# Kernel tuning notes

Measured on AMD Instinct MI355X. Metric: run time of the kernel, lower is better.

The kernel has to match this reference:

```python
import jax, jax.numpy as jnp
import numpy as np

N, E, F_IN, G = 50000, 800000, 128, 256
LAYERS = [(128, 4, 64), (256, 4, 64), (256, 1, 64)]  # (fan_in, heads, per-head dim)


def setup_inputs() -> dict:
    key = jax.random.key(0)
    ks = iter(jax.random.split(key, 64))
    nrm = lambda shp, s=1.0: jax.random.normal(next(ks), shp, jnp.float32) * s
    d = {}
    d["x"] = nrm((N, F_IN))
    d["edge_index"] = jax.random.randint(next(ks), (2, E), 0, N, dtype=jnp.int32)
    d["batch"] = jnp.sort(jax.random.randint(next(ks), (N,), 0, G, dtype=jnp.int32))
    for i, (fin, h, c) in enumerate(LAYERS):
        d[f"w{i}"] = nrm((fin, h * c), 1.0 / np.sqrt(fin))
        d[f"asrc{i}"] = nrm((h, c), 0.1)
        d[f"adst{i}"] = nrm((h, c), 0.1)
        d[f"b{i}"] = nrm((h * c,), 0.1)
        d[f"g{i}"] = 1.0 + nrm((h * c,), 0.1)
        d[f"be{i}"] = nrm((h * c,), 0.1)
        d[f"m{i}"] = nrm((h * c,), 0.1)
        d[f"v{i}"] = jnp.abs(nrm((h * c,), 0.1)) + 1.0
    d["fc1w"] = nrm((192, 64), 1.0 / np.sqrt(192)); d["fc1b"] = nrm((64,), 0.1)
    d["fc2w"] = nrm((64, 32), 1.0 / np.sqrt(64));   d["fc2b"] = nrm((32,), 0.1)
    d["fc3w"] = nrm((32, 1), 1.0 / np.sqrt(32));    d["fc3b"] = nrm((1,), 0.1)
    return d


def _gat_layer(x, w, a_s, a_d, b, src, dst, n, heads):
    c = w.shape[1] // heads
    h = (x @ w).reshape(n, heads, c)                      # [N,H,C]
    al_s = jnp.sum(h * a_s[None], axis=-1)                # [N,H]
    al_d = jnp.sum(h * a_d[None], axis=-1)                # [N,H]
    e = jax.nn.leaky_relu(al_s[src] + al_d[dst], 0.2)     # [E',H]
    emax = jax.ops.segment_max(e, dst, num_segments=n)
    emax = jnp.where(jnp.isfinite(emax), emax, 0.0)
    ee = jnp.exp(e - emax[dst])
    den = jax.ops.segment_sum(ee, dst, num_segments=n)
    alpha = ee / (den[dst] + 1e-16)                       # edge softmax per dst node
    out = jax.ops.segment_sum(h[src] * alpha[..., None], dst, num_segments=n)
    return out.reshape(n, heads * c) + b


def _bn(x, g, be, m, v):
    return (x - m) * jax.lax.rsqrt(v + 1e-5) * g + be


def reference(x, edge_index, batch,
              w0, asrc0, adst0, b0, g0, be0, m0, v0,
              w1, asrc1, adst1, b1, g1, be1, m1, v1,
              w2, asrc2, adst2, b2, g2, be2, m2, v2,
              fc1w, fc1b, fc2w, fc2b, fc3w, fc3b):
    n = x.shape[0]
    loop = jnp.arange(n, dtype=edge_index.dtype)          # add_self_loops (PyG default)
    src = jnp.concatenate([edge_index[0], loop])
    dst = jnp.concatenate([edge_index[1], loop])
    layers = [(w0, asrc0, adst0, b0, g0, be0, m0, v0, 4),
              (w1, asrc1, adst1, b1, g1, be1, m1, v1, 4),
              (w2, asrc2, adst2, b2, g2, be2, m2, v2, 1)]
    for (w, a_s, a_d, b, g, be, m, v, heads) in layers:
        x = _gat_layer(x, w, a_s, a_d, b, src, dst, n, heads)
        x = jax.nn.elu(_bn(x, g, be, m, v))
    # multi-pool readout over graphs
    xsum = jax.ops.segment_sum(x, batch, num_segments=G)
    cnt = jax.ops.segment_sum(jnp.ones((n, 1), x.dtype), batch, num_segments=G)
    xmean = xsum / jnp.maximum(cnt, 1.0)
    xmax = jax.ops.segment_max(x, batch, num_segments=G)
    xmax = jnp.where(jnp.isfinite(xmax), xmax, 0.0)
    h = jnp.concatenate([xmean, xmax, xsum], axis=1)      # [G, 192]
    h = jax.nn.relu(h @ fc1w + fc1b)
    h = jax.nn.relu(h @ fc2w + fc2b)
    return h @ fc3w + fc3b                                # [G, 1]
```

## Files before the change

kernel.cpp:

```cpp
#include <hip/hip_runtime.h>
#include <hip/hip_fp16.h>

typedef unsigned short ushort_t;
typedef unsigned int uint_t;
typedef __attribute__((ext_vector_type(8))) _Float16 half8;
typedef __attribute__((ext_vector_type(4))) float f32x4;

#define NN 50000
#define NE 800000
#define NGR 256
#define MAXDEG 64

#define FILL_GROUPS 196
#define FA_G 151

typedef __attribute__((address_space(3))) unsigned int as3_u32;
typedef const __attribute__((address_space(1))) unsigned int as1_u32c;
__device__ __forceinline__ void gld16(const ushort_t* g, void* lds_base) {
    __builtin_amdgcn_global_load_lds((as1_u32c*)g, (as3_u32*)lds_base, 16, 0, 0);
}

__device__ __forceinline__ void fill_body(int grp, int r,
                                          const int* __restrict__ esrc,
                                          const int* __restrict__ edst,
                                          int* __restrict__ deg,
                                          ushort_t* __restrict__ colv) {
    int base = grp * 4096 + (int)threadIdx.x * 4;
    int4 dv[4], sv[4];
    #pragma unroll
    for (int u = 0; u < 4; ++u) {
        int b = base + u * 1024;
        bool ok = b < NE;
        int bb = ok ? b : 0;
        dv[u] = *(const int4*)(edst + bb);
        sv[u] = *(const int4*)(esrc + bb);
        if (!ok) { dv[u].x = -1; dv[u].y = -1; dv[u].z = -1; dv[u].w = -1; }
    }
    const int lo = r * 6250;
    #pragma unroll
    for (int u = 0; u < 4; ++u) {
        const int* dp = (const int*)&dv[u];
        const int* sp = (const int*)&sv[u];
        #pragma unroll
        for (int j = 0; j < 4; ++j) {
            int d = dp[j];
            if ((unsigned)(d - lo) < 6250u) {
                int pos = atomicAdd(&deg[d], 1);
                if (pos < MAXDEG - 1) colv[(d << 6) + 1 + pos] = (ushort_t)sp[j];
            }
        }
    }
}

__global__ __launch_bounds__(256)
void k_pf1(const float* __restrict__ x0, __half* __restrict__ xf,
           const float* __restrict__ W0, const float* __restrict__ W1,
           const float* __restrict__ W2, __half* __restrict__ th,
           const int* __restrict__ esrc, const int* __restrict__ edst,
           int* __restrict__ deg, ushort_t* __restrict__ colv) {
    constexpr int FB1 = FA_G * 8;
    if (blockIdx.x < FB1) {
        fill_body(blockIdx.x >> 3, blockIdx.x & 7, esrc, edst, deg, colv);
    } else {
        int i = (blockIdx.x - FB1) * 256 + threadIdx.x;
        if (i < 1600000) {
            float4 v = ((const float4*)x0)[i];
            __half2 a = __floats2half2_rn(v.x, v.y);
            __half2 b = __floats2half2_rn(v.z, v.w);
            *(__half2*)(xf + i * 4) = a;
            *(__half2*)(xf + i * 4 + 2) = b;
        } else if (i < 1600000 + 114688) {
            int w = i - 1600000;
            const float* W; int K, NC, idx, base;
            if (w < 32768)      { W = W0; K = 128; NC = 256; idx = w;         base = 0; }
            else if (w < 98304) { W = W1; K = 256; NC = 256; idx = w - 32768; base = 32768; }
            else                { W = W2; K = 256; NC = 64;  idx = w - 98304; base = 98304; }
            int k = idx / NC, n = idx % NC;
            th[base + n * K + k] = __float2half(W[idx]);
        } else if (i < 1600000 + 114688 + NN) {
            int n = i - 1714688;
            colv[n << 6] = (ushort_t)n;
        }
    }
}

template<int KD, int BN>
__device__ __forceinline__ void gemm_body(int bx, int by,
    const __half* __restrict__ Ax, const __half* __restrict__ Bth,
    __half* __restrict__ Hout, const float* __restrict__ a_s,
    const float* __restrict__ a_d, float* __restrict__ als,
    float* __restrict__ ald, int H, int M, int NC) {
    constexpr int BM = 128, BK = 32;
    __shared__ ushort_t sA[BM * BK];
    __shared__ ushort_t sB[BN * BK];
    const int tid = threadIdx.x;
    const int m0 = bx * BM;
    const int n0 = by * BN;
    const int wv = tid >> 6, ln = tid & 63;
    const int lrow = ln & 15, lq = ln >> 4;
    constexpr int RT = (BN == 128) ? 4 : 2;
    int wm, wn;
    if constexpr (BN == 128) { wm = (wv >> 1) * 64; wn = (wv & 1) * 64; }
    else                     { wm = wv * 32;        wn = 0; }
    const int roff = ln >> 2;
    const int coff = (ln & 3) * 8;

    f32x4 acc[RT][4] = {};

    for (int k0 = 0; k0 < KD; k0 += BK) {
        #pragma unroll
        for (int ch = 0; ch < 2; ++ch) {
            int rb = wv * 32 + ch * 16;
            size_t ga = (size_t)(m0 + rb + roff) * KD + k0 + coff;
            gld16((const ushort_t*)Ax + ga, &sA[rb * BK]);
        }
        if constexpr (BN == 128) {
            #pragma unroll
            for (int ch = 0; ch < 2; ++ch) {
                int rb = wv * 32 + ch * 16;
                size_t gb = (size_t)(n0 + rb + roff) * KD + k0 + coff;
                gld16((const ushort_t*)Bth + gb, &sB[rb * BK]);
            }
        } else {
            int rb = wv * 16;
            size_t gb = (size_t)(n0 + rb + roff) * KD + k0 + coff;
            gld16((const ushort_t*)Bth + gb, &sB[rb * BK]);
        }
        __syncthreads();
        half8 af[RT], bf[4];
        #pragma unroll
        for (int r = 0; r < RT; ++r)
            af[r] = *(const half8*)&sA[(wm + r * 16 + lrow) * BK + lq * 8];
        #pragma unroll
        for (int c = 0; c < 4; ++c)
            bf[c] = *(const half8*)&sB[(wn + c * 16 + lrow) * BK + lq * 8];
        #pragma unroll
        for (int r = 0; r < RT; ++r)
            #pragma unroll
            for (int c = 0; c < 4; ++c)
                acc[r][c] = __builtin_amdgcn_mfma_f32_16x16x32_f16(af[r], bf[c], acc[r][c], 0, 0, 0);
        __syncthreads();
    }
    #pragma unroll
    for (int r = 0; r < RT; ++r) {
        #pragma unroll
        for (int c = 0; c < 4; ++c) {
            int colg = n0 + wn + c * 16 + lrow;
            #pragma unroll
            for (int j = 0; j < 4; ++j) {
                int row = m0 + wm + r * 16 + lq * 4 + j;
                if (row < M) Hout[(size_t)row * NC + colg] = __float2half(acc[r][c][j]);
            }
        }
    }
    int hh = (n0 + wn) >> 6;
    float asv[4], adv[4];
    #pragma unroll
    for (int c = 0; c < 4; ++c) {
        int cg = (n0 + wn + c * 16 + lrow) & 63;
        asv[c] = a_s[hh * 64 + cg];
        adv[c] = a_d[hh * 64 + cg];
    }
    #pragma unroll
    for (int r = 0; r < RT; ++r) {
        #pragma unroll
        for (int j = 0; j < 4; ++j) {
            float ts = 0.f, td = 0.f;
            #pragma unroll
            for (int c = 0; c < 4; ++c) {
                float v = acc[r][c][j];
                ts += v * asv[c];
                td += v * adv[c];
            }
            #pragma unroll
            for (int m = 1; m < 16; m <<= 1) {
                ts += __shfl_xor(ts, m);
                td += __shfl_xor(td, m);
            }
            int row = m0 + wm + r * 16 + lq * 4 + j;
            if (lrow == 0 && row < M) {
                als[row * H + hh] = ts;
                ald[row * H + hh] = td;
            }
        }
    }
}

template<int KD, int BN>
__global__ __launch_bounds__(256)
void k_mgemm(const __half* __restrict__ Ax, const __half* __restrict__ Bth,
             __half* __restrict__ Hout,
             const float* __restrict__ a_s, const float* __restrict__ a_d,
             float* __restrict__ als, float* __restrict__ ald,
             int H, int M, int NC) {
    gemm_body<KD, BN>(blockIdx.x, blockIdx.y, Ax, Bth, Hout, a_s, a_d, als, ald, H, M, NC);
}

__global__ __launch_bounds__(256)
void k_pf2(const __half* __restrict__ Ax, const __half* __restrict__ Bth,
           __half* __restrict__ Hout,
           const float* __restrict__ a_s, const float* __restrict__ a_d,
           float* __restrict__ als, float* __restrict__ ald, int M,
           const int* __restrict__ esrc, const int* __restrict__ edst,
           int* __restrict__ deg, ushort_t* __restrict__ colv) {
    constexpr int FB2 = (FILL_GROUPS - FA_G) * 8;
    if (blockIdx.x < FB2) {
        fill_body(FA_G + (blockIdx.x >> 3), blockIdx.x & 7, esrc, edst, deg, colv);
    } else {
        int g = blockIdx.x - FB2;
        gemm_body<128, 128>(g >> 1, g & 1, Ax, Bth, Hout,
                            a_s, a_d, als, ald, 4, M, 256);
    }
}

__global__ __launch_bounds__(256)
void k_fagg4s(const __half* __restrict__ h, const float* __restrict__ als,
              const float* __restrict__ ald, const int* __restrict__ deg,
              const ushort_t* __restrict__ colv,
              const float* __restrict__ bias, const float* __restrict__ gam,
              const float* __restrict__ bet, const float* __restrict__ mu,
              const float* __restrict__ var,
              __half* __restrict__ xo, int M) {
    __shared__ uint_t wraw[4][64];
    int wv = threadIdx.x >> 6;
    int half = blockIdx.x & 1;
    int node = (blockIdx.x >> 1) * 4 + wv;
    if (node >= M) return;
    int l = threadIdx.x & 63;
    int dg = deg[node] + 1;
    if (dg > MAXDEG) dg = MAXDEG;
    int rs = node << 6;

    float2 ad = *(const float2*)(ald + (size_t)node * 4 + half * 2);
    bool vld = l < dg;
    int s = (int)colv[vld ? rs + l : rs];
    int cv = s;
    float2 av = *(const float2*)((const char*)als + ((size_t)(uint_t)s << 4) + half * 8);
    float e0 = av.x + ad.x; e0 = e0 > 0.f ? e0 : 0.2f * e0; e0 = vld ? __expf(e0) : 0.f;
    float e1 = av.y + ad.y; e1 = e1 > 0.f ? e1 : 0.2f * e1; e1 = vld ? __expf(e1) : 0.f;
    float d0 = e0, d1 = e1;
    __half2 p = __floats2half2_rn(e0, e1);
    wraw[wv][l] = *(uint_t*)&p;
    #pragma unroll
    for (int off = 1; off < 64; off <<= 1) {
        d0 += __shfl_xor(d0, off); d1 += __shfl_xor(d1, off);
    }

    float a0 = 0.f, a1 = 0.f;
    const uint_t shB = (uint_t)((l & 32) >> 1);
    const uint_t loffB = (uint_t)(half * 256 + l * 4);
    int nrem = dg;
    #pragma unroll
    for (int grp = 0; grp < 3; ++grp) {
        int g0 = grp * 24;
        if (g0 < nrem) {
            uint_t hu[3][8];
            #pragma unroll
            for (int bb = 0; bb < 3; ++bb) {
                if (g0 + bb * 8 < nrem) {
                    #pragma unroll
                    for (int u = 0; u < 8; ++u) {
                        int sv = __builtin_amdgcn_readlane(cv, g0 + bb * 8 + u);
                        const char* hp = (const char*)h + ((size_t)(uint_t)sv << 9);
                        hu[bb][u] = *(const uint_t*)(hp + loffB);
                    }
                }
            }
            #pragma unroll
            for (int bb = 0; bb < 3; ++bb) {
                if (g0 + bb * 8 < nrem) {
                    #pragma unroll
                    for (int u = 0; u < 8; ++u) {
                        int j = g0 + bb * 8 + u;
                        uint_t w = wraw[wv][j];
                        uint_t afv = w >> shB;
                        asm("v_fma_mix_f32 %0, %1, %2, %0 op_sel:[0,0,0] op_sel_hi:[1,1,0]"
                            : "+v"(a0) : "v"(afv), "v"(hu[bb][u]));
                        asm("v_fma_mix_f32 %0, %1, %2, %0 op_sel:[0,1,0] op_sel_hi:[1,1,0]"
                            : "+v"(a1) : "v"(afv), "v"(hu[bb][u]));
                    }
                }
            }
        }
    }

    float den = (l & 32) ? d1 : d0;
    float inv = 1.f / (den + 1e-16f);
    int chg = half * 128 + l * 2;
    float2 bi = *(const float2*)(bias + chg);
    float2 ga = *(const float2*)(gam + chg);
    float2 be = *(const float2*)(bet + chg);
    float2 m2 = *(const float2*)(mu + chg);
    float2 v2 = *(const float2*)(var + chg);
    float o0 = a0 * inv + bi.x;
    float o1 = a1 * inv + bi.y;
    float bn0 = (o0 - m2.x) * rsqrtf(v2.x + 1e-5f) * ga.x + be.x;
    float bn1 = (o1 - m2.y) * rsqrtf(v2.y + 1e-5f) * ga.y + be.y;
    float f0 = bn0 > 0.f ? bn0 : (__expf(bn0) - 1.f);
    float f1 = bn1 > 0.f ? bn1 : (__expf(bn1) - 1.f);
    __half2 pk = __floats2half2_rn(f0, f1);
    *(uint_t*)&xo[(size_t)node * 256 + chg] = *(uint_t*)&pk;
}

__global__ __launch_bounds__(256)
void k_fagg1(const __half* __restrict__ h, const float* __restrict__ als,
             const float* __restrict__ ald, const int* __restrict__ deg,
             const ushort_t* __restrict__ colv,
             const float* __restrict__ bias, const float* __restrict__ gam,
             const float* __restrict__ bet, const float* __restrict__ mu,
             const float* __restrict__ var,
             float* __restrict__ xf, int M) {
    __shared__ uint_t wraw[4][64];
    int node = blockIdx.x * 4 + (threadIdx.x >> 6);
    if (node >= M) return;
    int wv = (threadIdx.x >> 6) & 3;
    int l = threadIdx.x & 63;
    int dg = deg[node] + 1;
    if (dg > MAXDEG) dg = MAXDEG;
    int rs = node << 6;

    float ad = ald[node];
    bool vld = l < dg;
    int s = (int)colv[vld ? rs + l : rs];
    int cv = s;
    float e = als[s] + ad; e = e > 0.f ? e : 0.2f * e; e = vld ? __expf(e) : 0.f;
    float d0 = e;
    wraw[wv][l] = __float_as_uint(e);
    #pragma unroll
    for (int off = 1; off < 64; off <<= 1) d0 += __shfl_xor(d0, off);

    float a0 = 0.f;
    int nrem = dg;
    #pragma unroll
    for (int grp = 0; grp < 3; ++grp) {
        int g0 = grp * 24;
        if (g0 < nrem) {
            uint_t hu[3][8];
            #pragma unroll
            for (int bb = 0; bb < 3; ++bb) {
                if (g0 + bb * 8 < nrem) {
                    #pragma unroll
                    for (int u = 0; u < 8; ++u) {
                        int sv = __builtin_amdgcn_readlane(cv, g0 + bb * 8 + u);
                        const ushort_t* hp = (const ushort_t*)h + ((size_t)(uint_t)sv << 6);
                        hu[bb][u] = (uint_t)hp[l];
                    }
                }
            }
            #pragma unroll
            for (int bb = 0; bb < 3; ++bb) {
                if (g0 + bb * 8 < nrem) {
                    #pragma unroll
                    for (int u = 0; u < 8; ++u) {
                        int j = g0 + bb * 8 + u;
                        uint_t wfv = wraw[wv][j];
                        asm("v_fma_mix_f32 %0, %1, %2, %0 op_sel:[0,0,0] op_sel_hi:[0,1,0]"
                            : "+v"(a0) : "v"(wfv), "v"(hu[bb][u]));
                    }
                }
            }
        }
    }

    float inv = 1.f / (d0 + 1e-16f);
    float o = a0 * inv + bias[l];
    float bn = (o - mu[l]) * rsqrtf(var[l] + 1e-5f) * gam[l] + bet[l];
    float fo = bn > 0.f ? bn : (__expf(bn) - 1.f);
    xf[(size_t)node * 64 + l] = fo;
}

__global__ __launch_bounds__(512)
void k_poolfc(const float* __restrict__ x, const int* __restrict__ batch,
              const float* __restrict__ fc1w, const float* __restrict__ fc1b,
              const float* __restrict__ fc2w, const float* __restrict__ fc2b,
              const float* __restrict__ fc3w, const float* __restrict__ fc3b,
              float* __restrict__ out, int M) {
    __shared__ float ssum[8][64];
    __shared__ float smax[8][64];
    __shared__ float hb[192];
    __shared__ float h1[64];
    __shared__ float h2[32];
    int g = blockIdx.x, t = threadIdx.x;
    int d = t & 63, sub = t >> 6;
    int lo = 0, hi = M;
    while (lo < hi) { int mid = (lo + hi) >> 1; if (batch[mid] < g) lo = mid + 1; else hi = mid; }
    int s = lo;
    lo = 0; hi = M;
    while (lo < hi) { int mid = (lo + hi) >> 1; if (batch[mid] < g + 1) lo = mid + 1; else hi = mid; }
    int e = lo;
    float sum = 0.f, mx = -3.0e38f;
    for (int n = s + sub; n < e; n += 8) {
        float v = x[(size_t)n * 64 + d];
        sum += v; mx = fmaxf(mx, v);
    }
    ssum[sub][d] = sum; smax[sub][d] = mx;
    __syncthreads();
    if (t < 64) {
        float sm = 0.f, m2 = -3.0e38f;
        #pragma unroll
        for (int k = 0; k < 8; ++k) { sm += ssum[k][t]; m2 = fmaxf(m2, smax[k][t]); }
        int cnt = e - s;
        hb[t] = sm / (float)(cnt > 1 ? cnt : 1);
        hb[64 + t] = (cnt == 0) ? 0.f : m2;
        hb[128 + t] = sm;
    }
    __syncthreads();
    if (t < 64) {
        float s1 = fc1b[t];
        for (int k = 0; k < 192; ++k) s1 += hb[k] * fc1w[k * 64 + t];
        h1[t] = fmaxf(s1, 0.f);
    }
    __syncthreads();
    if (t < 32) {
        float s2 = fc2b[t];
        for (int k = 0; k < 64; ++k) s2 += h1[k] * fc2w[k * 32 + t];
        h2[t] = fmaxf(s2, 0.f);
    }
    __syncthreads();
    if (t == 0) {
        float s3 = fc3b[0];
        for (int k = 0; k < 32; ++k) s3 += h2[k] * fc3w[k];
        out[g] = s3;
    }
}

extern "C" void kernel_launch(void* const* d_in, const int* in_sizes, int n_in,
                              void* d_out, int out_size, void* d_ws, size_t ws_size,
                              hipStream_t stream) {
    const float* x0     = (const float*)d_in[0];
    const int* ei       = (const int*)d_in[1];
    const int* batch    = (const int*)d_in[2];
    const float* W[3]   = {(const float*)d_in[3],  (const float*)d_in[11], (const float*)d_in[19]};
    const float* AS[3]  = {(const float*)d_in[4],  (const float*)d_in[12], (const float*)d_in[20]};
    const float* AD[3]  = {(const float*)d_in[5],  (const float*)d_in[13], (const float*)d_in[21]};
    const float* BI[3]  = {(const float*)d_in[6],  (const float*)d_in[14], (const float*)d_in[22]};
    const float* GA[3]  = {(const float*)d_in[7],  (const float*)d_in[15], (const float*)d_in[23]};
    const float* BE[3]  = {(const float*)d_in[8],  (const float*)d_in[16], (const float*)d_in[24]};
    const float* MU[3]  = {(const float*)d_in[9],  (const float*)d_in[17], (const float*)d_in[25]};
    const float* VA[3]  = {(const float*)d_in[10], (const float*)d_in[18], (const float*)d_in[26]};
    const float* fc1w = (const float*)d_in[27];
    const float* fc1b = (const float*)d_in[28];
    const float* fc2w = (const float*)d_in[29];
    const float* fc2b = (const float*)d_in[30];
    const float* fc3w = (const float*)d_in[31];
    const float* fc3b = (const float*)d_in[32];

    char* ws = (char*)d_ws;
    ushort_t* colv = (ushort_t*)(ws);
    int*   deg    = (int*)  (ws + 6400000);
    float* als    = (float*)(ws + 6600192);
    float* ald    = (float*)(ws + 7400192);
    __half* wTh   = (__half*)(ws + 8200192);
    __half* h_buf = (__half*)(ws + 8429568);
    __half* xf16  = (__half*)(ws + 34029568);
    float* xpool  = (float*)(ws + 59654144);

    const int* esrc = ei;
    const int* edst = ei + NE;

    const int GB = (NN + 127) / 128;
    const int FB1 = FA_G * 8;
    const int FB2 = (FILL_GROUPS - FA_G) * 8;
    const int PREPB = (1600000 + 114688 + NN + 255) / 256;
    int nwb = (NN + 3) / 4;
    int nsb = nwb * 2;

    hipMemsetAsync(deg, 0, NN * sizeof(int), stream);

    k_pf1<<<FB1 + PREPB, 256, 0, stream>>>(x0, xf16, W[0], W[1], W[2], wTh,
                                           esrc, edst, deg, colv);
    k_pf2<<<FB2 + 782, 256, 0, stream>>>(xf16, wTh, h_buf, AS[0], AD[0], als, ald, NN,
                                         esrc, edst, deg, colv);

    k_fagg4s<<<nsb, 256, 0, stream>>>(h_buf, als, ald, deg, colv,
                                      BI[0], GA[0], BE[0], MU[0], VA[0], xf16, NN);
    k_mgemm<256, 128><<<dim3(GB, 2), 256, 0, stream>>>(xf16, wTh + 32768, h_buf,
                                                       AS[1], AD[1], als, ald, 4, NN, 256);
    k_fagg4s<<<nsb, 256, 0, stream>>>(h_buf, als, ald, deg, colv,
                                      BI[1], GA[1], BE[1], MU[1], VA[1], xf16, NN);
    k_mgemm<256, 64><<<dim3(GB, 1), 256, 0, stream>>>(xf16, wTh + 98304, h_buf,
                                                      AS[2], AD[2], als, ald, 1, NN, 64);
    k_fagg1<<<nwb, 256, 0, stream>>>(h_buf, als, ald, deg, colv,
                                     BI[2], GA[2], BE[2], MU[2], VA[2], xpool, NN);

    k_poolfc<<<NGR, 512, 0, stream>>>(xpool, batch, fc1w, fc1b, fc2w, fc2b, fc3w, fc3b,
                                      (float*)d_out, NN);
    (void)in_sizes; (void)n_in; (void)out_size; (void)ws_size;
}
```

Before: 387.7 us.

## Overlap second half of layer-0 aggregation with first rows of layer-1 GEMM

Splits the layer-0 aggregation at node NSPLIT: the first half runs alone, then a fused kernel runs the second half of the aggregation alongside layer-1 GEMM row-blocks that only read the already-finished first half. The remaining GEMM rows run in a separate launch. Layer-1 outputs go to new double-buffered h/als/ald workspace so the GEMM does not overwrite data the concurrent aggregation still reads. The aim is to fill the device during the aggregation tail and hide part of the GEMM, at the cost of an extra launch and more workspace.

```diff
diff --git a/kernel.cpp b/kernel.cpp
--- a/kernel.cpp
+++ b/kernel.cpp
@@ -13,6 +13,8 @@
 
 #define FILL_GROUPS 196
 #define FA_G 151
+
+#define NSPLIT 25088
 
 typedef __attribute__((address_space(3))) unsigned int as3_u32;
 typedef const __attribute__((address_space(1))) unsigned int as1_u32c;
@@ -196,6 +198,17 @@
     gemm_body<KD, BN>(blockIdx.x, blockIdx.y, Ax, Bth, Hout, a_s, a_d, als, ald, H, M, NC);
 }
 
+template<int KD, int BN>
+__global__ __launch_bounds__(256)
+void k_mgemmL(const __half* __restrict__ Ax, const __half* __restrict__ Bth,
+              __half* __restrict__ Hout,
+              const float* __restrict__ a_s, const float* __restrict__ a_d,
+              float* __restrict__ als, float* __restrict__ ald,
+              int H, int M, int NC, int bx_base) {
+    gemm_body<KD, BN>(bx_base + ((int)blockIdx.x >> 1), blockIdx.x & 1,
+                      Ax, Bth, Hout, a_s, a_d, als, ald, H, M, NC);
+}
+
 __global__ __launch_bounds__(256)
 void k_pf2(const __half* __restrict__ Ax, const __half* __restrict__ Bth,
            __half* __restrict__ Hout,
@@ -213,8 +226,8 @@
     }
 }
 
-__global__ __launch_bounds__(256)
-void k_fagg4s(const __half* __restrict__ h, const float* __restrict__ als,
+__device__ __forceinline__ void fagg4s_body(int bid, int node_base,
+              const __half* __restrict__ h, const float* __restrict__ als,
               const float* __restrict__ ald, const int* __restrict__ deg,
               const ushort_t* __restrict__ colv,
               const float* __restrict__ bias, const float* __restrict__ gam,
@@ -223,8 +236,8 @@
               __half* __restrict__ xo, int M) {
     __shared__ uint_t wraw[4][64];
     int wv = threadIdx.x >> 6;
-    int half = blockIdx.x & 1;
-    int node = (blockIdx.x >> 1) * 4 + wv;
+    int half = bid & 1;
+    int node = node_base + (bid >> 1) * 4 + wv;
     if (node >= M) return;
     int l = threadIdx.x & 63;
     int dg = deg[node] + 1;
@@ -300,6 +313,40 @@
     float f1 = bn1 > 0.f ? bn1 : (__expf(bn1) - 1.f);
     __half2 pk = __floats2half2_rn(f0, f1);
     *(uint_t*)&xo[(size_t)node * 256 + chg] = *(uint_t*)&pk;
+}
+
+__global__ __launch_bounds__(256)
+void k_fagg4s(const __half* __restrict__ h, const float* __restrict__ als,
+              const float* __restrict__ ald, const int* __restrict__ deg,
+              const ushort_t* __restrict__ colv,
+              const float* __restrict__ bias, const float* __restrict__ gam,
+              const float* __restrict__ bet, const float* __restrict__ mu,
+              const float* __restrict__ var,
+              __half* __restrict__ xo, int M, int node_base) {
+    fagg4s_body(blockIdx.x, node_base, h, als, ald, deg, colv,
+                bias, gam, bet, mu, var, xo, M);
+}
+
+__global__ __launch_bounds__(256)
+void k_fg(const __half* __restrict__ hA, const float* __restrict__ alsA,
+          const float* __restrict__ aldA, const int* __restrict__ deg,
+          const ushort_t* __restrict__ colv,
+          const float* __restrict__ bias, const float* __restrict__ gam,
+          const float* __restrict__ bet, const float* __restrict__ mu,
+          const float* __restrict__ var, __half* __restrict__ xo,
+          const __half* __restrict__ Ax, const __half* __restrict__ Bth,
+          __half* __restrict__ HoutB,
+          const float* __restrict__ a_s, const float* __restrict__ a_d,
+          float* __restrict__ alsB, float* __restrict__ aldB, int M) {
+    constexpr int FGB = 2 * ((NN - NSPLIT) / 4);
+    if (blockIdx.x < FGB) {
+        fagg4s_body(blockIdx.x, NSPLIT, hA, alsA, aldA, deg, colv,
+                    bias, gam, bet, mu, var, xo, M);
+    } else {
+        int g = blockIdx.x - FGB;
+        gemm_body<256, 128>(g >> 1, g & 1, Ax, Bth, HoutB,
+                            a_s, a_d, alsB, aldB, 4, M, 256);
+    }
 }
 
 __global__ __launch_bounds__(256)
@@ -448,12 +495,15 @@
     char* ws = (char*)d_ws;
     ushort_t* colv = (ushort_t*)(ws);
     int*   deg    = (int*)  (ws + 6400000);
-    float* als    = (float*)(ws + 6600192);
-    float* ald    = (float*)(ws + 7400192);
+    float* alsA   = (float*)(ws + 6600192);
+    float* aldA   = (float*)(ws + 7400192);
     __half* wTh   = (__half*)(ws + 8200192);
-    __half* h_buf = (__half*)(ws + 8429568);
+    __half* h_bufA= (__half*)(ws + 8429568);
     __half* xf16  = (__half*)(ws + 34029568);
     float* xpool  = (float*)(ws + 59654144);
+    __half* h_bufB= (__half*)(ws + 72454144);
+    float* alsB   = (float*)(ws + 98054144);
+    float* aldB   = (float*)(ws + 98854144);
 
     const int* esrc = ei;
     const int* edst = ei + NE;
@@ -462,6 +512,8 @@
     const int FB1 = FA_G * 8;
     const int FB2 = (FILL_GROUPS - FA_G) * 8;
     const int PREPB = (1600000 + 114688 + NN + 255) / 256;
+    const int FAGA = 2 * (NSPLIT / 4);
+    const int FAGB = 2 * ((NN - NSPLIT) / 4);
     int nwb = (NN + 3) / 4;
     int nsb = nwb * 2;
 
@@ -469,18 +521,22 @@
 
     k_pf1<<<FB1 + PREPB, 256, 0, stream>>>(x0, xf16, W[0], W[1], W[2], wTh,
                                            esrc, edst, deg, colv);
-    k_pf2<<<FB2 + 782, 256, 0, stream>>>(xf16, wTh, h_buf, AS[0], AD[0], als, ald, NN,
+    k_pf2<<<FB2 + 782, 256, 0, stream>>>(xf16, wTh, h_bufA, AS[0], AD[0], alsA, aldA, NN,
                                          esrc, edst, deg, colv);
 
-    k_fagg4s<<<nsb, 256, 0, stream>>>(h_buf, als, ald, deg, colv,
-                                      BI[0], GA[0], BE[0], MU[0], VA[0], xf16, NN);
-    k_mgemm<256, 128><<<dim3(GB, 2), 256, 0, stream>>>(xf16, wTh + 32768, h_buf,
-                                                       AS[1], AD[1], als, ald, 4, NN, 256);
-    k_fagg4s<<<nsb, 256, 0, stream>>>(h_buf, als, ald, deg, colv,
-                                      BI[1], GA[1], BE[1], MU[1], VA[1], xf16, NN);
-    k_mgemm<256, 64><<<dim3(GB, 1), 256, 0, stream>>>(xf16, wTh + 98304, h_buf,
-                                                      AS[2], AD[2], als, ald, 1, NN, 64);
-    k_fagg1<<<nwb, 256, 0, stream>>>(h_buf, als, ald, deg, colv,
+    k_fagg4s<<<FAGA, 256, 0, stream>>>(h_bufA, alsA, aldA, deg, colv,
+                                       BI[0], GA[0], BE[0], MU[0], VA[0], xf16, NN, 0);
+    k_fg<<<FAGB + 392, 256, 0, stream>>>(h_bufA, alsA, aldA, deg, colv,
+                                         BI[0], GA[0], BE[0], MU[0], VA[0], xf16,
+                                         xf16, wTh + 32768, h_bufB, AS[1], AD[1],
+                                         alsB, aldB, NN);
+    k_mgemmL<256, 128><<<390, 256, 0, stream>>>(xf16, wTh + 32768, h_bufB,
+                                                AS[1], AD[1], alsB, aldB, 4, NN, 256, 196);
+    k_fagg4s<<<nsb, 256, 0, stream>>>(h_bufB, alsB, aldB, deg, colv,
+                                      BI[1], GA[1], BE[1], MU[1], VA[1], xf16, NN, 0);
+    k_mgemm<256, 64><<<dim3(GB, 1), 256, 0, stream>>>(xf16, wTh + 98304, h_bufA,
+                                                      AS[2], AD[2], alsA, aldA, 1, NN, 64);
+    k_fagg1<<<nwb, 256, 0, stream>>>(h_bufA, alsA, aldA, deg, colv,
                                      BI[2], GA[2], BE[2], MU[2], VA[2], xpool, NN);
 
     k_poolfc<<<NGR, 512, 0, stream>>>(xpool, batch, fc1w, fc1b, fc2w, fc2b, fc3w, fc3b,
```

After: 438.4 us. +13.1%, slower.
